# Optimization experiments

Measured on AMD Instinct MI355X. Metric: run time of the kernel, lower is better.

## Reference

```python
import jax, jax.numpy as jnp
import numpy as np

# Static configuration (from init_kwargs)
B, T, SP = 4, 100, 20          # batch, max_time_patches, max_space_patches
S = T * SP                      # flattened seq len = 2000
H, NH = 512, 8                  # hidden size, heads
D = H // NH                     # head dim = 64
CF, CB = 4, 4                   # context_forward, context_backward
ROPE_BASE = 10000.0
NEG = -1e9


def setup_inputs() -> dict:
    key = jax.random.key(0)
    ks = jax.random.split(key, 8)
    w = 1.0 / np.sqrt(H)
    x = jax.random.normal(ks[0], (B, S, H), jnp.float32)
    # token order is space-major: timestamps = time-patch id repeated per space patch
    timestamps = jnp.broadcast_to(jnp.tile(jnp.arange(T, dtype=jnp.int32), SP), (B, S))
    attn_mask = jnp.ones((B, S), jnp.int32)
    Wq = jax.random.normal(ks[1], (H, H), jnp.float32) * w
    Wk = jax.random.normal(ks[2], (H, H), jnp.float32) * w
    Wv = jax.random.normal(ks[3], (H, H), jnp.float32) * w
    Wo = jax.random.normal(ks[4], (H, H), jnp.float32) * w
    z = jnp.zeros((H,), jnp.float32)
    return {"x": x, "attn_mask": attn_mask, "timestamps": timestamps,
            "Wq": Wq, "bq": z, "Wk": Wk, "bk": z, "Wv": Wv, "bv": z,
            "Wo": Wo, "bo": z}


def _rotate_half(u):
    return jnp.concatenate((-u[..., D // 2:], u[..., :D // 2]), axis=-1)


def _rope_tables():
    inv_freq = 1.0 / (ROPE_BASE ** (jnp.arange(0, D, 2, dtype=jnp.float32) / D))
    t = jnp.arange(T, dtype=jnp.float32)
    freqs = t[:, None] * inv_freq[None, :]          # [T, D/2]
    emb = jnp.concatenate((freqs, freqs), axis=-1)  # [T, D]
    return jnp.cos(emb), jnp.sin(emb)


def _context_mask():
    # forward/backward banded window in time, tiled over space patches
    ones = jnp.ones((T, T), jnp.float32)
    m = jnp.triu(ones, k=-CF).T          # allow up to CF future time patches
    if CB > 0:
        m = m * jnp.triu(ones, k=-CB)    # allow up to CB past time patches
    return jnp.tile(m, (SP, SP))         # [S, S]


def reference(x, attn_mask, timestamps, Wq, bq, Wk, bk, Wv, bv, Wo, bo):
    # projections -> [B, NH, S, D]
    def heads(w, b):
        return (x @ w + b).reshape(B, S, NH, D).transpose(0, 2, 1, 3)
    q, k, v = heads(Wq, bq), heads(Wk, bk), heads(Wv, bv)

    # rotary position embedding indexed by time-patch timestamps
    cos_t, sin_t = _rope_tables()
    cos = cos_t[timestamps][:, None]     # [B, 1, S, D]
    sin = sin_t[timestamps][:, None]
    q = q * cos + _rotate_half(q) * sin
    k = k * cos + _rotate_half(k) * sin

    # banded-context masked attention
    scores = jnp.einsum('bhqd,bhkd->bhqk', q, k) / jnp.sqrt(jnp.float32(D))
    mask = (_context_mask()[None, None, :, :] *
            attn_mask[:, None, None, :].astype(jnp.float32)) > 0
    scores = jnp.where(mask, scores, NEG)
    attn = jax.nn.softmax(scores, axis=-1)
    out = jnp.einsum('bhqk,bhkd->bhqd', attn, v)
    out = out.transpose(0, 2, 1, 3).reshape(B, S, H)
    return out @ Wo + bo
```

## Files before the change

### kernel.cpp

```cpp
#include <hip/hip_runtime.h>
#include <hip/hip_bf16.h>
#include <stdint.h>


typedef __bf16 bf16x8 __attribute__((ext_vector_type(8)));
typedef float f32x4 __attribute__((ext_vector_type(4)));

static const size_t O_XB = 0;
static const size_t O_WT = 8192000;
static const size_t O_Q  = 10289152;
static const size_t O_K  = 18481152;
static const size_t O_V  = 26673152;
static const size_t O_RC = 34865152;
static const size_t O_RS = 34877952;
static const size_t O_VT = 34890752;

__device__ inline void gload16(const void* g, void* l) {
  __builtin_amdgcn_global_load_lds((const __attribute__((address_space(1))) void*)g,
                                   (__attribute__((address_space(3))) void*)l, 16, 0, 0);
}

__device__ inline int xcd_swz(int orig, int nwg) {
  const int q8 = nwg >> 3, r8 = nwg & 7;
  const int xcd = orig & 7;
  return (xcd < r8 ? xcd * (q8 + 1) : r8 * (q8 + 1) + (xcd - r8) * q8) + (orig >> 3);
}

__global__ __launch_bounds__(256) void prep_kernel(
    const float* __restrict__ x, const float* __restrict__ Wq, const float* __restrict__ Wk,
    const float* __restrict__ Wv, const float* __restrict__ Wo,
    __bf16* __restrict__ xb, __bf16* __restrict__ wt,
    float* __restrict__ ropeC, float* __restrict__ ropeS)
{
  __shared__ float tile[64][65];
  const int tid = threadIdx.x;
  const int bx = blockIdx.x;
  if (bx < 4000) {
    const int idx = bx * 256 + tid;
    float4 v = ((const float4*)x)[idx];
    union { ushort4 u; __bf16 b[4]; } p;
    p.b[0] = (__bf16)v.x; p.b[1] = (__bf16)v.y; p.b[2] = (__bf16)v.z; p.b[3] = (__bf16)v.w;
    ((ushort4*)xb)[idx] = p.u;
    return;
  }
  const int wb = bx - 4000;
  const int mat = wb >> 6, sub = wb & 63;
  const int tk = (sub >> 3) * 64, tn = (sub & 7) * 64;
  const float* W = (mat == 0) ? Wq : (mat == 1) ? Wk : (mat == 2) ? Wv : Wo;
#pragma unroll
  for (int it = 0; it < 16; ++it) {
    const int idx = it * 256 + tid;
    const int kl = idx >> 6, nl = idx & 63;
    tile[kl][nl] = W[(size_t)(tk + kl) * 512 + tn + nl];
  }
  __syncthreads();
#pragma unroll
  for (int it = 0; it < 16; ++it) {
    const int idx = it * 256 + tid;
    const int nl = idx >> 6, kl = idx & 63;
    wt[(size_t)mat * 262144 + (size_t)(tn + nl) * 512 + tk + kl] = (__bf16)tile[kl][nl];
  }
  if (wb == 0) {
    for (int idx = tid; idx < 3200; idx += 256) {
      const int t = idx >> 5, i = idx & 31;
      const float f = (float)t * powf(10000.0f, -(float)i / 32.0f);
      ropeC[idx] = cosf(f);
      ropeS[idx] = sinf(f);
    }
  }
}

__device__ inline void gemm_core_db(const __bf16* __restrict__ A, const __bf16* __restrict__ Bm,
                                    __bf16* As, __bf16* Bs, f32x4 (&acc)[4][4],
                                    int m0, int n0, int tid, int wm, int wn, int lr, int g)
{
  const int r0 = tid >> 2;
  const int aq = tid & 3;
  int gm0 = m0 + r0;      if (gm0 > 7999) gm0 = 7999;
  int gm1 = m0 + r0 + 64; if (gm1 > 7999) gm1 = 7999;
  const __bf16* a0 = A + (size_t)gm0 * 512 + aq * 8;
  const __bf16* a1 = A + (size_t)gm1 * 512 + aq * 8;
  const __bf16* b0 = Bm + (size_t)(n0 + r0) * 512 + aq * 8;
  const __bf16* b1 = Bm + (size_t)(n0 + r0 + 64) * 512 + aq * 8;

  gload16(a0, As + tid * 8);
  gload16(a1, As + tid * 8 + 2048);
  gload16(b0, Bs + tid * 8);
  gload16(b1, Bs + tid * 8 + 2048);
  asm volatile("s_waitcnt vmcnt(0)" ::: "memory");
  __syncthreads();

  int cur = 0;
  for (int kk = 0; kk < 512; kk += 32) {
    const int nxt = cur ^ 1;
    if (kk + 32 < 512) {
      gload16(a0 + kk + 32, As + nxt * 4096 + tid * 8);
      gload16(a1 + kk + 32, As + nxt * 4096 + tid * 8 + 2048);
      gload16(b0 + kk + 32, Bs + nxt * 4096 + tid * 8);
      gload16(b1 + kk + 32, Bs + nxt * 4096 + tid * 8 + 2048);
    }
    bf16x8 af[4], bfr[4];
#pragma unroll
    for (int f = 0; f < 4; ++f) {
      af[f]  = *(const bf16x8*)(As + cur * 4096 + (wm + f * 16 + lr) * 32 + g * 8);
      bfr[f] = *(const bf16x8*)(Bs + cur * 4096 + (wn + f * 16 + lr) * 32 + g * 8);
    }
#pragma unroll
    for (int i = 0; i < 4; ++i)
#pragma unroll
      for (int j = 0; j < 4; ++j)
        acc[i][j] = __builtin_amdgcn_mfma_f32_16x16x32_bf16(af[i], bfr[j], acc[i][j], 0, 0, 0);
    if (kk + 32 < 512)
      asm volatile("s_waitcnt vmcnt(0)" ::: "memory");
    __syncthreads();
    cur = nxt;
  }
}

__global__ __launch_bounds__(256) void qkv_gemm(
    const __bf16* __restrict__ xb, const __bf16* __restrict__ wt,
    const float* __restrict__ bq, const float* __restrict__ bk, const float* __restrict__ bv,
    const float* __restrict__ ropeC, const float* __restrict__ ropeS,
    __bf16* __restrict__ qws, __bf16* __restrict__ kws, __bf16* __restrict__ vws)
{
  const int tid = threadIdx.x;
  const int wgid = xcd_swz(blockIdx.x, 756);
  const int mt = wgid / 12;
  const int rest = wgid - mt * 12;
  const int mat = rest >> 2;
  const int nt = rest & 3;
  const int m0 = mt * 128, n0 = nt * 128;
  __shared__ __bf16 As[8192], Bs[8192];
  f32x4 acc[4][4] = {};
  const int wid = tid >> 6, lane = tid & 63;
  const int wm = (wid >> 1) << 6, wn = (wid & 1) << 6;
  const int lr = lane & 15, g = lane >> 4;

  gemm_core_db(xb, wt + (size_t)mat * 262144, As, Bs, acc, m0, n0, tid, wm, wn, lr, g);

  const int hn = (n0 + wn) >> 6;
  const float* bias = (mat == 0) ? bq : (mat == 1) ? bk : bv;
  __bf16* outp = (mat == 0) ? qws : (mat == 1) ? kws : vws;
  const float qscale = (mat == 0) ? 0.125f : 1.0f;

#pragma unroll
  for (int i = 0; i < 4; ++i) {
#pragma unroll
    for (int r = 0; r < 4; ++r) {
      const int m = m0 + wm + i * 16 + g * 4 + r;
      if (m >= 8000) continue;
      const int b = m / 2000;
      const int s = m - b * 2000;
      const int t = s % 100;
      const int sp = s / 100;
      const int pos = t * 20 + sp;
      const size_t ob = ((size_t)(b * 8 + hn) * 2000 + pos) * 64;
      if (mat == 2) {
#pragma unroll
        for (int j = 0; j < 4; ++j) {
          float v = acc[i][j][r] + bias[n0 + wn + j * 16 + lr];
          outp[ob + j * 16 + lr] = (__bf16)v;
        }
      } else {
#pragma unroll
        for (int j = 0; j < 2; ++j) {
          const int dlo = j * 16 + lr;
          const float alo = acc[i][j][r]     + bias[n0 + wn + j * 16 + lr];
          const float ahi = acc[i][j + 2][r] + bias[n0 + wn + (j + 2) * 16 + lr];
          const float cs = ropeC[t * 32 + dlo], sn = ropeS[t * 32 + dlo];
          const float olo = (alo * cs - ahi * sn) * qscale;
          const float ohi = (ahi * cs + alo * sn) * qscale;
          outp[ob + dlo]      = (__bf16)olo;
          outp[ob + dlo + 32] = (__bf16)ohi;
        }
      }
    }
  }
}

__global__ __launch_bounds__(256) void vt_transpose(
    const __bf16* __restrict__ v, __bf16* __restrict__ vt)
{
  __shared__ __align__(16) __bf16 tile[64][68];
  const int tid = threadIdx.x;
  const int p0 = blockIdx.x * 64;
  const int bh = blockIdx.y;
  const __bf16* vp = v + (size_t)bh * 2000 * 64;
  __bf16* vtp = vt + (size_t)bh * 64 * 2000;
  const int np = (p0 + 64 <= 2000) ? 64 : (2000 - p0);

#pragma unroll
  for (int it = 0; it < 4; ++it) {
    const int idx = it * 256 + tid;
    const int pl = idx >> 4, d4 = (idx & 15) * 4;
    if (pl < np) {
      const ushort4 u = *(const ushort4*)(vp + (size_t)(p0 + pl) * 64 + d4);
      *(ushort4*)&tile[pl][d4] = u;
    }
  }
  __syncthreads();
#pragma unroll
  for (int it = 0; it < 16; ++it) {
    const int idx = it * 256 + tid;
    const int d = idx >> 6, p = idx & 63;
    if (p < np) vtp[(size_t)d * 2000 + p0 + p] = tile[p][d];
  }
}

__global__ __launch_bounds__(256) void attn_kernel(
    const __bf16* __restrict__ qw, const __bf16* __restrict__ kw, const __bf16* __restrict__ vt,
    const int* __restrict__ amask, __bf16* __restrict__ aout)
{
  const int wid = threadIdx.x >> 6, lane = threadIdx.x & 63;
  const int lr = lane & 15, g = lane >> 4;
  const int tq = blockIdx.x * 4 + wid;
  const int h = blockIdx.y, b = blockIdx.z;

  int t0 = tq - 4; if (t0 < 0) t0 = 0;
  int t1 = tq + 4; if (t1 > 99) t1 = 99;
  const int k0 = t0 * 20;
  const int nk = (t1 - t0 + 1) * 20;
  const int base = k0 & ~7;

  __shared__ __bf16 Pl[4][20][200];
  __shared__ float addm[4][192];

  const size_t hb = (size_t)(b * 8 + h) * 2000;
  const __bf16* qp = qw + (hb + (size_t)tq * 20) * 64;
  const __bf16* vtp = vt + (size_t)(b * 8 + h) * 64 * 2000;

  for (int k = lane; k < 192; k += 64) {
    const int kg = base + k;
    float v = -1e9f;
    if (kg >= k0 && kg < k0 + nk) {
      const int tk = kg / 20;
      const int spk = kg - tk * 20;
      if (amask[b * 2000 + spk * 100 + tk] != 0) v = 0.0f;
    }
    addm[wid][k] = v;
  }

  bf16x8 qf[2][2];
#pragma unroll
  for (int jq = 0; jq < 2; ++jq) {
    int q = jq * 16 + lr; if (q > 19) q = 19;
#pragma unroll
    for (int ks = 0; ks < 2; ++ks)
      qf[jq][ks] = *(const bf16x8*)(qp + q * 64 + ks * 32 + g * 8);
  }

  f32x4 acc[12][2] = {};
  __builtin_amdgcn_s_setprio(1);
#pragma unroll
  for (int i = 0; i < 12; ++i) {
    int krow = base + i * 16 + lr; if (krow > 1999) krow = 1999;
    const __bf16* kr = kw + (hb + (size_t)krow) * 64;
    const bf16x8 af0 = *(const bf16x8*)(kr + g * 8);
    const bf16x8 af1 = *(const bf16x8*)(kr + 32 + g * 8);
    acc[i][0] = __builtin_amdgcn_mfma_f32_16x16x32_bf16(af0, qf[0][0], acc[i][0], 0, 0, 0);
    acc[i][0] = __builtin_amdgcn_mfma_f32_16x16x32_bf16(af1, qf[0][1], acc[i][0], 0, 0, 0);
    acc[i][1] = __builtin_amdgcn_mfma_f32_16x16x32_bf16(af0, qf[1][0], acc[i][1], 0, 0, 0);
    acc[i][1] = __builtin_amdgcn_mfma_f32_16x16x32_bf16(af1, qf[1][1], acc[i][1], 0, 0, 0);
  }
  __builtin_amdgcn_s_setprio(0);

  __syncthreads();

#pragma unroll
  for (int jq = 0; jq < 2; ++jq) {
    float mx = -1e30f;
#pragma unroll
    for (int i = 0; i < 12; ++i)
#pragma unroll
      for (int r = 0; r < 4; ++r) {
        acc[i][jq][r] += addm[wid][i * 16 + g * 4 + r];
        mx = fmaxf(mx, acc[i][jq][r]);
      }
    mx = fmaxf(mx, __shfl_xor(mx, 16));
    mx = fmaxf(mx, __shfl_xor(mx, 32));
    float sm = 0.0f;
#pragma unroll
    for (int i = 0; i < 12; ++i)
#pragma unroll
      for (int r = 0; r < 4; ++r) {
        const float p = __expf(acc[i][jq][r] - mx);
        acc[i][jq][r] = p;
        sm += p;
      }
    sm += __shfl_xor(sm, 16);
    sm += __shfl_xor(sm, 32);
    const float rinv = 1.0f / sm;
    const int q = jq * 16 + lr;
    if (q < 20) {
#pragma unroll
      for (int i = 0; i < 12; ++i) {
        union { ushort4 u; __bf16 e[4]; } pk;
        pk.e[0] = (__bf16)(acc[i][jq][0] * rinv);
        pk.e[1] = (__bf16)(acc[i][jq][1] * rinv);
        pk.e[2] = (__bf16)(acc[i][jq][2] * rinv);
        pk.e[3] = (__bf16)(acc[i][jq][3] * rinv);
        *(ushort4*)&Pl[wid][q][i * 16 + g * 4] = pk.u;
      }
    }
  }

  __syncthreads();

  f32x4 acc2[2][4] = {};
  __builtin_amdgcn_s_setprio(1);
#pragma unroll
  for (int kb = 0; kb < 6; ++kb) {
    int kv = base + kb * 32 + g * 8; if (kv >= 2000) kv = 0;
    bf16x8 bfv[4];
#pragma unroll
    for (int j2 = 0; j2 < 4; ++j2)
      bfv[j2] = *(const bf16x8*)(vtp + (size_t)(j2 * 16 + lr) * 2000 + kv);
#pragma unroll
    for (int i2 = 0; i2 < 2; ++i2) {
      int qr = i2 * 16 + lr; if (qr > 19) qr = 19;
      const bf16x8 pa = *(const bf16x8*)&Pl[wid][qr][kb * 32 + g * 8];
#pragma unroll
      for (int j2 = 0; j2 < 4; ++j2)
        acc2[i2][j2] = __builtin_amdgcn_mfma_f32_16x16x32_bf16(pa, bfv[j2], acc2[i2][j2], 0, 0, 0);
    }
  }
  __builtin_amdgcn_s_setprio(0);

#pragma unroll
  for (int i2 = 0; i2 < 2; ++i2)
#pragma unroll
    for (int r = 0; r < 4; ++r) {
      const int q = i2 * 16 + g * 4 + r;
      if (q < 20) {
        const size_t ob = ((size_t)b * 2000 + q * 100 + tq) * 512 + h * 64;
#pragma unroll
        for (int j2 = 0; j2 < 4; ++j2)
          aout[ob + j2 * 16 + lr] = (__bf16)acc2[i2][j2][r];
      }
    }
}

__global__ __launch_bounds__(256) void out_gemm(
    const __bf16* __restrict__ ab, const __bf16* __restrict__ wot,
    const float* __restrict__ bo, float* __restrict__ out)
{
  const int tid = threadIdx.x;
  const int wgid = xcd_swz(blockIdx.x, 252);
  const int mt = wgid >> 2, nt = wgid & 3;
  const int m0 = mt * 128, n0 = nt * 128;
  __shared__ __bf16 As[8192], Bs[8192];
  f32x4 acc[4][4] = {};
  const int wid = tid >> 6, lane = tid & 63;
  const int wm = (wid >> 1) << 6, wn = (wid & 1) << 6;
  const int lr = lane & 15, g = lane >> 4;

  gemm_core_db(ab, wot, As, Bs, acc, m0, n0, tid, wm, wn, lr, g);

#pragma unroll
  for (int i = 0; i < 4; ++i) {
#pragma unroll
    for (int r = 0; r < 4; ++r) {
      const int m = m0 + wm + i * 16 + g * 4 + r;
      if (m < 8000) {
#pragma unroll
        for (int j = 0; j < 4; ++j) {
          const int n = n0 + wn + j * 16 + lr;
          out[(size_t)m * 512 + n] = acc[i][j][r] + bo[n];
        }
      }
    }
  }
}

extern "C" void kernel_launch(void* const* d_in, const int* in_sizes, int n_in,
                              void* d_out, int out_size, void* d_ws, size_t ws_size,
                              hipStream_t stream) {
  const float* x   = (const float*)d_in[0];
  const int* amask = (const int*)d_in[1];
  const float* Wq = (const float*)d_in[3];
  const float* bq = (const float*)d_in[4];
  const float* Wk = (const float*)d_in[5];
  const float* bk = (const float*)d_in[6];
  const float* Wv = (const float*)d_in[7];
  const float* bv = (const float*)d_in[8];
  const float* Wo = (const float*)d_in[9];
  const float* bo = (const float*)d_in[10];
  float* out = (float*)d_out;

  char* ws = (char*)d_ws;
  __bf16* xb    = (__bf16*)(ws + O_XB);
  __bf16* wt    = (__bf16*)(ws + O_WT);
  __bf16* qws   = (__bf16*)(ws + O_Q);
  __bf16* kws   = (__bf16*)(ws + O_K);
  __bf16* vws   = (__bf16*)(ws + O_V);
  float*  ropeC = (float*)(ws + O_RC);
  float*  ropeS = (float*)(ws + O_RS);
  __bf16* vtw   = (__bf16*)(ws + O_VT);
  __bf16* aout  = (__bf16*)(ws + O_XB);

  prep_kernel<<<4256, 256, 0, stream>>>(x, Wq, Wk, Wv, Wo, xb, wt, ropeC, ropeS);
  qkv_gemm<<<756, 256, 0, stream>>>(xb, wt, bq, bk, bv, ropeC, ropeS, qws, kws, vws);
  vt_transpose<<<dim3(32, 32), 256, 0, stream>>>(vws, vtw);
  attn_kernel<<<dim3(25, 8, 4), 256, 0, stream>>>(qws, kws, vtw, amask, aout);
  out_gemm<<<252, 256, 0, stream>>>(aout, wt + 3 * 262144, bo, out);
}
```

Measured before the change: 89.55 us.

## Triple-buffer GEMM K-loop, precompute row positions, fuse V transpose into attention

The shared GEMM core moves from a double-buffered loop with full vmcnt(0) waits to a three-stage LDS pipeline that prefetches two K-slices ahead and waits only for the oldest loads. The QKV epilogue now reads per-row destination offsets and timestamps from a small shared table instead of doing integer divisions per element. The separate V-transpose kernel is removed: each attention block loads its V window straight from the V buffer and transposes it into shared memory. This saves one launch and a global round trip, at the cost of more LDS per GEMM and attention block and scalar bank-conflicting transposed LDS writes.

```diff
diff --git a/kernel.cpp b/kernel.cpp
--- a/kernel.cpp
+++ b/kernel.cpp
@@ -13,7 +13,6 @@
 static const size_t O_V  = 26673152;
 static const size_t O_RC = 34865152;
 static const size_t O_RS = 34877952;
-static const size_t O_VT = 34890752;
 
 __device__ inline void gload16(const void* g, void* l) {
   __builtin_amdgcn_global_load_lds((const __attribute__((address_space(1))) void*)g,
@@ -70,7 +69,23 @@
   }
 }
 
-__device__ inline void gemm_core_db(const __bf16* __restrict__ A, const __bf16* __restrict__ Bm,
+__device__ inline void mfma_step(const __bf16* ab, const __bf16* bb,
+                                 f32x4 (&acc)[4][4], int wm, int wn, int lr, int g)
+{
+  bf16x8 af[4], bfr[4];
+#pragma unroll
+  for (int f = 0; f < 4; ++f) {
+    af[f]  = *(const bf16x8*)(ab + (wm + f * 16 + lr) * 32 + g * 8);
+    bfr[f] = *(const bf16x8*)(bb + (wn + f * 16 + lr) * 32 + g * 8);
+  }
+#pragma unroll
+  for (int i = 0; i < 4; ++i)
+#pragma unroll
+    for (int j = 0; j < 4; ++j)
+      acc[i][j] = __builtin_amdgcn_mfma_f32_16x16x32_bf16(af[i], bfr[j], acc[i][j], 0, 0, 0);
+}
+
+__device__ inline void gemm_core_p2(const __bf16* __restrict__ A, const __bf16* __restrict__ Bm,
                                     __bf16* As, __bf16* Bs, f32x4 (&acc)[4][4],
                                     int m0, int n0, int tid, int wm, int wn, int lr, int g)
 {
@@ -83,38 +98,33 @@
   const __bf16* b0 = Bm + (size_t)(n0 + r0) * 512 + aq * 8;
   const __bf16* b1 = Bm + (size_t)(n0 + r0 + 64) * 512 + aq * 8;
 
-  gload16(a0, As + tid * 8);
-  gload16(a1, As + tid * 8 + 2048);
-  gload16(b0, Bs + tid * 8);
-  gload16(b1, Bs + tid * 8 + 2048);
+#define STAGE_QK(J, BUF) do {                                      \
+    gload16(a0 + (J) * 32, As + (BUF) * 4096 + tid * 8);           \
+    gload16(a1 + (J) * 32, As + (BUF) * 4096 + tid * 8 + 2048);    \
+    gload16(b0 + (J) * 32, Bs + (BUF) * 4096 + tid * 8);           \
+    gload16(b1 + (J) * 32, Bs + (BUF) * 4096 + tid * 8 + 2048);    \
+  } while (0)
+
+  STAGE_QK(0, 0);
+  STAGE_QK(1, 1);
+  __syncthreads();
+
+  int cur = 0, st = 2;
+  for (int k = 0; k < 14; ++k) {
+    STAGE_QK(k + 2, st);
+    mfma_step(As + cur * 4096, Bs + cur * 4096, acc, wm, wn, lr, g);
+    asm volatile("s_waitcnt vmcnt(4)" ::: "memory");
+    __builtin_amdgcn_s_barrier();
+    __builtin_amdgcn_sched_barrier(0);
+    if (++cur == 3) cur = 0;
+    if (++st == 3) st = 0;
+  }
+  mfma_step(As + 2 * 4096, Bs + 2 * 4096, acc, wm, wn, lr, g);
   asm volatile("s_waitcnt vmcnt(0)" ::: "memory");
-  __syncthreads();
-
-  int cur = 0;
-  for (int kk = 0; kk < 512; kk += 32) {
-    const int nxt = cur ^ 1;
-    if (kk + 32 < 512) {
-      gload16(a0 + kk + 32, As + nxt * 4096 + tid * 8);
-      gload16(a1 + kk + 32, As + nxt * 4096 + tid * 8 + 2048);
-      gload16(b0 + kk + 32, Bs + nxt * 4096 + tid * 8);
-      gload16(b1 + kk + 32, Bs + nxt * 4096 + tid * 8 + 2048);
-    }
-    bf16x8 af[4], bfr[4];
-#pragma unroll
-    for (int f = 0; f < 4; ++f) {
-      af[f]  = *(const bf16x8*)(As + cur * 4096 + (wm + f * 16 + lr) * 32 + g * 8);
-      bfr[f] = *(const bf16x8*)(Bs + cur * 4096 + (wn + f * 16 + lr) * 32 + g * 8);
-    }
-#pragma unroll
-    for (int i = 0; i < 4; ++i)
-#pragma unroll
-      for (int j = 0; j < 4; ++j)
-        acc[i][j] = __builtin_amdgcn_mfma_f32_16x16x32_bf16(af[i], bfr[j], acc[i][j], 0, 0, 0);
-    if (kk + 32 < 512)
-      asm volatile("s_waitcnt vmcnt(0)" ::: "memory");
-    __syncthreads();
-    cur = nxt;
-  }
+  __builtin_amdgcn_s_barrier();
+  __builtin_amdgcn_sched_barrier(0);
+  mfma_step(As, Bs, acc, wm, wn, lr, g);
+#undef STAGE_QK
 }
 
 __global__ __launch_bounds__(256) void qkv_gemm(
@@ -130,13 +140,23 @@
   const int mat = rest >> 2;
   const int nt = rest & 3;
   const int m0 = mt * 128, n0 = nt * 128;
-  __shared__ __bf16 As[8192], Bs[8192];
+  __shared__ __bf16 As[12288], Bs[12288];
+  __shared__ int posTbl[128];
   f32x4 acc[4][4] = {};
   const int wid = tid >> 6, lane = tid & 63;
   const int wm = (wid >> 1) << 6, wn = (wid & 1) << 6;
   const int lr = lane & 15, g = lane >> 4;
 
-  gemm_core_db(xb, wt + (size_t)mat * 262144, As, Bs, acc, m0, n0, tid, wm, wn, lr, g);
+  if (tid < 128) {
+    int m = m0 + tid; if (m > 7999) m = 7999;
+    const int b = m / 2000;
+    const int s = m - b * 2000;
+    const int t = s % 100;
+    const int sp = s / 100;
+    posTbl[tid] = ((b * 16000 + t * 20 + sp) << 7) | t;
+  }
+
+  gemm_core_p2(xb, wt + (size_t)mat * 262144, As, Bs, acc, m0, n0, tid, wm, wn, lr, g);
 
   const int hn = (n0 + wn) >> 6;
   const float* bias = (mat == 0) ? bq : (mat == 1) ? bk : bv;
@@ -147,14 +167,12 @@
   for (int i = 0; i < 4; ++i) {
 #pragma unroll
     for (int r = 0; r < 4; ++r) {
-      const int m = m0 + wm + i * 16 + g * 4 + r;
+      const int row = wm + i * 16 + g * 4 + r;
+      const int m = m0 + row;
       if (m >= 8000) continue;
-      const int b = m / 2000;
-      const int s = m - b * 2000;
-      const int t = s % 100;
-      const int sp = s / 100;
-      const int pos = t * 20 + sp;
-      const size_t ob = ((size_t)(b * 8 + hn) * 2000 + pos) * 64;
+      const int pk = posTbl[row];
+      const int t = pk & 127;
+      const size_t ob = ((size_t)((pk >> 7) + hn * 2000)) * 64;
       if (mat == 2) {
 #pragma unroll
         for (int j = 0; j < 4; ++j) {
@@ -178,40 +196,12 @@
   }
 }
 
-__global__ __launch_bounds__(256) void vt_transpose(
-    const __bf16* __restrict__ v, __bf16* __restrict__ vt)
-{
-  __shared__ __align__(16) __bf16 tile[64][68];
+__global__ __launch_bounds__(256) void attn_kernel(
+    const __bf16* __restrict__ qw, const __bf16* __restrict__ kw, const __bf16* __restrict__ vw,
+    const int* __restrict__ amask, __bf16* __restrict__ aout)
+{
+  const int wid = threadIdx.x >> 6, lane = threadIdx.x & 63;
   const int tid = threadIdx.x;
-  const int p0 = blockIdx.x * 64;
-  const int bh = blockIdx.y;
-  const __bf16* vp = v + (size_t)bh * 2000 * 64;
-  __bf16* vtp = vt + (size_t)bh * 64 * 2000;
-  const int np = (p0 + 64 <= 2000) ? 64 : (2000 - p0);
-
-#pragma unroll
-  for (int it = 0; it < 4; ++it) {
-    const int idx = it * 256 + tid;
-    const int pl = idx >> 4, d4 = (idx & 15) * 4;
-    if (pl < np) {
-      const ushort4 u = *(const ushort4*)(vp + (size_t)(p0 + pl) * 64 + d4);
-      *(ushort4*)&tile[pl][d4] = u;
-    }
-  }
-  __syncthreads();
-#pragma unroll
-  for (int it = 0; it < 16; ++it) {
-    const int idx = it * 256 + tid;
-    const int d = idx >> 6, p = idx & 63;
-    if (p < np) vtp[(size_t)d * 2000 + p0 + p] = tile[p][d];
-  }
-}
-
-__global__ __launch_bounds__(256) void attn_kernel(
-    const __bf16* __restrict__ qw, const __bf16* __restrict__ kw, const __bf16* __restrict__ vt,
-    const int* __restrict__ amask, __bf16* __restrict__ aout)
-{
-  const int wid = threadIdx.x >> 6, lane = threadIdx.x & 63;
   const int lr = lane & 15, g = lane >> 4;
   const int tq = blockIdx.x * 4 + wid;
   const int h = blockIdx.y, b = blockIdx.z;
@@ -220,17 +210,25 @@
   int t1 = tq + 4; if (t1 > 99) t1 = 99;
   const int k0 = t0 * 20;
   const int nk = (t1 - t0 + 1) * 20;
-  const int base = k0 & ~7;
-
+  const int basew = k0 & ~7;
+
+  const int tq0 = blockIdx.x * 4;
+  int t0b = tq0 - 4; if (t0b < 0) t0b = 0;
+  int t1b = tq0 + 7; if (t1b > 99) t1b = 99;
+  const int kb0 = (t0b * 20) & ~7;
+  const int nks = (t1b + 1) * 20 - kb0;
+  const int woff = basew - kb0;
+
+  __shared__ __bf16 Vs[64][264];
   __shared__ __bf16 Pl[4][20][200];
   __shared__ float addm[4][192];
 
   const size_t hb = (size_t)(b * 8 + h) * 2000;
   const __bf16* qp = qw + (hb + (size_t)tq * 20) * 64;
-  const __bf16* vtp = vt + (size_t)(b * 8 + h) * 64 * 2000;
+  const __bf16* vp = vw + (hb + (size_t)kb0) * 64;
 
   for (int k = lane; k < 192; k += 64) {
-    const int kg = base + k;
+    const int kg = basew + k;
     float v = -1e9f;
     if (kg >= k0 && kg < k0 + nk) {
       const int tk = kg / 20;
@@ -240,6 +238,17 @@
     addm[wid][k] = v;
   }
 
+  for (int idx = tid; idx < 264 * 16; idx += 256) {
+    const int pr = idx >> 4, d4 = (idx & 15) * 4;
+    union { ushort4 u; __bf16 e[4]; } p;
+    p.u = make_ushort4(0, 0, 0, 0);
+    if (pr < nks) p.u = *(const ushort4*)(vp + (size_t)pr * 64 + d4);
+    Vs[d4 + 0][pr] = p.e[0];
+    Vs[d4 + 1][pr] = p.e[1];
+    Vs[d4 + 2][pr] = p.e[2];
+    Vs[d4 + 3][pr] = p.e[3];
+  }
+
   bf16x8 qf[2][2];
 #pragma unroll
   for (int jq = 0; jq < 2; ++jq) {
@@ -253,7 +262,7 @@
   __builtin_amdgcn_s_setprio(1);
 #pragma unroll
   for (int i = 0; i < 12; ++i) {
-    int krow = base + i * 16 + lr; if (krow > 1999) krow = 1999;
+    int krow = basew + i * 16 + lr; if (krow > 1999) krow = 1999;
     const __bf16* kr = kw + (hb + (size_t)krow) * 64;
     const bf16x8 af0 = *(const bf16x8*)(kr + g * 8);
     const bf16x8 af1 = *(const bf16x8*)(kr + 32 + g * 8);
@@ -310,11 +319,11 @@
   __builtin_amdgcn_s_setprio(1);
 #pragma unroll
   for (int kb = 0; kb < 6; ++kb) {
-    int kv = base + kb * 32 + g * 8; if (kv >= 2000) kv = 0;
+    const int kvloc = woff + kb * 32 + g * 8;
     bf16x8 bfv[4];
 #pragma unroll
     for (int j2 = 0; j2 < 4; ++j2)
-      bfv[j2] = *(const bf16x8*)(vtp + (size_t)(j2 * 16 + lr) * 2000 + kv);
+      bfv[j2] = *(const bf16x8*)&Vs[j2 * 16 + lr][kvloc];
 #pragma unroll
     for (int i2 = 0; i2 < 2; ++i2) {
       int qr = i2 * 16 + lr; if (qr > 19) qr = 19;
@@ -348,13 +357,13 @@
   const int wgid = xcd_swz(blockIdx.x, 252);
   const int mt = wgid >> 2, nt = wgid & 3;
   const int m0 = mt * 128, n0 = nt * 128;
-  __shared__ __bf16 As[8192], Bs[8192];
+  __shared__ __bf16 As[12288], Bs[12288];
   f32x4 acc[4][4] = {};
   const int wid = tid >> 6, lane = tid & 63;
   const int wm = (wid >> 1) << 6, wn = (wid & 1) << 6;
   const int lr = lane & 15, g = lane >> 4;
 
-  gemm_core_db(ab, wot, As, Bs, acc, m0, n0, tid, wm, wn, lr, g);
+  gemm_core_p2(ab, wot, As, Bs, acc, m0, n0, tid, wm, wn, lr, g);
 
 #pragma unroll
   for (int i = 0; i < 4; ++i) {
@@ -395,12 +404,10 @@
   __bf16* vws   = (__bf16*)(ws + O_V);
   float*  ropeC = (float*)(ws + O_RC);
   float*  ropeS = (float*)(ws + O_RS);
-  __bf16* vtw   = (__bf16*)(ws + O_VT);
   __bf16* aout  = (__bf16*)(ws + O_XB);
 
   prep_kernel<<<4256, 256, 0, stream>>>(x, Wq, Wk, Wv, Wo, xb, wt, ropeC, ropeS);
   qkv_gemm<<<756, 256, 0, stream>>>(xb, wt, bq, bk, bv, ropeC, ropeS, qws, kws, vws);
-  vt_transpose<<<dim3(32, 32), 256, 0, stream>>>(vws, vtw);
-  attn_kernel<<<dim3(25, 8, 4), 256, 0, stream>>>(qws, kws, vtw, amask, aout);
+  attn_kernel<<<dim3(25, 8, 4), 256, 0, stream>>>(qws, kws, vws, amask, aout);
   out_gemm<<<252, 256, 0, stream>>>(aout, wt + 3 * 262144, bo, out);
 }
```

After: 88.08 us. About the same (-1.6%).
